# Optimization experiments

Measured on AMD Instinct MI355X. Metric: run time of the kernel, lower is better.

Reference implementation:

```python
import jax, jax.numpy as jnp
import numpy as np

LATENT = 100
INIT_SIZE = 8   # img_size // 4
NUM = 200       # LIF time steps
BETA = 0.95
THR = 1.0
CH_OUT = 3

# snntorch ATan surrogate spike (alpha=2 -> grad = 1/(1+(pi*u)^2))
@jax.custom_vjp
def spike_fn(x):
    return (x > 0).astype(x.dtype)

def _spike_fwd(x):
    return (x > 0).astype(x.dtype), x

def _spike_bwd(x, g):
    return (g / (1.0 + (jnp.pi * x) ** 2),)

spike_fn.defvjp(_spike_fwd, _spike_bwd)

def batchnorm(x, gamma, beta, eps):
    # training-mode BN: batch statistics over (N,H,W), biased variance (as torch)
    mean = x.mean(axis=(0, 2, 3), keepdims=True)
    var = ((x - mean) ** 2).mean(axis=(0, 2, 3), keepdims=True)
    xh = (x - mean) * jax.lax.rsqrt(var + eps)
    return xh * gamma[None, :, None, None] + beta[None, :, None, None]

def upsample2x(x):  # nearest-neighbor, scale 2
    return jnp.repeat(jnp.repeat(x, 2, axis=2), 2, axis=3)

def conv2d(x, w, b):  # 3x3, stride 1, padding 1
    y = jax.lax.conv_general_dilated(x, w, (1, 1), [(1, 1), (1, 1)],
                                     dimension_numbers=("NCHW", "OIHW", "NCHW"))
    return y + b[None, :, None, None]

def leaky_relu(x):
    return jnp.where(x >= 0, x, 0.2 * x)

def setup_inputs() -> dict:
    key = jax.random.key(0)
    ks = jax.random.split(key, 8)
    B = 8
    def n(k, shape, s=0.02):
        return jax.random.normal(k, shape, dtype=jnp.float32) * s
    return {
        "z": jax.random.normal(ks[0], (B, LATENT), dtype=jnp.float32),
        "w_l1": n(ks[1], (LATENT, 128 * INIT_SIZE ** 2)),
        "b_l1": jnp.zeros((128 * INIT_SIZE ** 2,), jnp.float32),
        "g1": jnp.ones((128,), jnp.float32), "be1": jnp.zeros((128,), jnp.float32),
        "w_c1": n(ks[2], (128, NUM * 128, 3, 3), 0.005),
        "b_c1": jnp.zeros((128,), jnp.float32),
        "g2": jnp.ones((128,), jnp.float32), "be2": jnp.zeros((128,), jnp.float32),
        "w_c2": n(ks[3], (64, 128, 3, 3)),
        "b_c2": jnp.zeros((64,), jnp.float32),
        "g3": jnp.ones((64,), jnp.float32), "be3": jnp.zeros((64,), jnp.float32),
        "w_c3": n(ks[4], (CH_OUT, 64, 3, 3)),
        "b_c3": jnp.zeros((CH_OUT,), jnp.float32),
    }

def reference(z, w_l1, b_l1, g1, be1, w_c1, b_c1, g2, be2, w_c2, b_c2, g3, be3, w_c3, b_c3):
    B = z.shape[0]
    out = z @ w_l1 + b_l1                       # (B, 128*8*8)
    out = out.reshape(B, 128, INIT_SIZE, INIT_SIZE)
    out = batchnorm(out, g1, be1, 1e-5)
    out = upsample2x(out)                       # (B,128,16,16) constant LIF input

    def lif_step(mem, _):
        # snntorch Leaky, reset-by-subtraction; reset detached from grad
        reset = jax.lax.stop_gradient((mem > THR).astype(mem.dtype))
        mem = BETA * mem + out - reset * THR
        spk = spike_fn(mem - THR)
        return mem, spk

    mem0 = jnp.zeros_like(out)
    _, spk_rec = jax.lax.scan(lif_step, mem0, None, length=NUM)  # (NUM,B,128,16,16)
    # faithful to torch.stack(dim=0).reshape(B, -1, 16, 16)
    x = spk_rec.reshape(B, NUM * 128, 16, 16)
    x = conv2d(x, w_c1, b_c1)                   # (B,128,16,16)
    x = leaky_relu(batchnorm(x, g2, be2, 0.8))  # BatchNorm2d(128, 0.8): eps=0.8
    x = upsample2x(x)                           # (B,128,32,32)
    x = conv2d(x, w_c2, b_c2)                   # (B,64,32,32)
    x = leaky_relu(batchnorm(x, g3, be3, 0.8))
    x = conv2d(x, w_c3, b_c3)                   # (B,3,32,32)
    return jnp.tanh(x)
```

## Files before the change

### kernel.cpp

```cpp
#include <hip/hip_runtime.h>
#include <math.h>


#define WROW 25632
#define SROW 25664

typedef _Float16 half8 __attribute__((ext_vector_type(8)));
typedef float f32x4 __attribute__((ext_vector_type(4)));
typedef unsigned int uint4v __attribute__((ext_vector_type(4)));

union AFrag { uint4v u4; unsigned int u[4]; half8 h; };

__global__ __launch_bounds__(256) void k_lin_bn1(
    const float* __restrict__ z, const float* __restrict__ w,
    const float* __restrict__ bias, const float* __restrict__ g1,
    const float* __restrict__ be1, float* __restrict__ I) {
  int ch = blockIdx.x, tid = threadIdx.x;
  __shared__ float red[256];
  int hw = tid & 63, b0 = tid >> 6;
  int j = ch * 64 + hw;
  float acc0 = bias[j], acc1 = acc0;
  const float* zp0 = z + b0 * 100;
  const float* zp1 = z + (b0 + 4) * 100;
  for (int l = 0; l < 100; ++l) {
    float wv = w[l * 8192 + j];
    acc0 += zp0[l] * wv;
    acc1 += zp1[l] * wv;
  }
  float v0 = acc0, v1 = acc1;
  red[tid] = v0 + v1; __syncthreads();
  for (int s = 128; s > 0; s >>= 1) { if (tid < s) red[tid] += red[tid + s]; __syncthreads(); }
  float mean = red[0] * (1.0f / 512.0f);
  __syncthreads();
  float d0 = v0 - mean, d1 = v1 - mean;
  red[tid] = d0 * d0 + d1 * d1; __syncthreads();
  for (int s = 128; s > 0; s >>= 1) { if (tid < s) red[tid] += red[tid + s]; __syncthreads(); }
  float var = red[0] * (1.0f / 512.0f);
  float coef = g1[ch] / sqrtf(var + 1e-5f);
  float beta = be1[ch];
  float q0 = (v0 - mean) * coef + beta;
  float q1 = (v1 - mean) * coef + beta;
#pragma unroll
  for (int k = 0; k < 2; ++k) {
    int n = k ? (tid + 256) : tid; float q = k ? q1 : q0;
    int b = n >> 6, hh = n & 63, h = hh >> 3, ww = hh & 7;
    float* o = I + (size_t)(b * 128 + ch) * 256 + (2 * h) * 16 + 2 * ww;
    o[0] = q; o[1] = q; o[16] = q; o[17] = q;
  }
}

__global__ __launch_bounds__(256) void k_lif(
    const float* __restrict__ I, unsigned char* __restrict__ spkTb) {
  int g = blockIdx.x * 256 + threadIdx.x;
  if (g < 217600) {
    int hr = g / 3200;
    int i  = g - hr * 3200;
    int row;
    if (hr < 18)      row = hr;
    else if (hr < 36) row = 306 + (hr - 18);
    else { int kk = hr - 36; row = ((kk >> 1) + 1) * 18 + ((kk & 1) ? 17 : 0); }
    *(unsigned long long*)(spkTb + (size_t)row * SROW + (size_t)i * 8) = 0ULL;
  }
  int px = g >> 10, plane = g & 1023;
  int lane = threadIdx.x & 63;
  float in = I[plane * 256 + px];
  int pos = ((px >> 4) + 1) * 18 + (px & 15) + 1;
  unsigned long long* wsrow =
      (unsigned long long*)(spkTb + (size_t)pos * SROW + ((plane - lane) >> 3));
  float mem = 0.0f;
  for (int t = 0; t < 200; ++t) {
    float reset = (mem > 1.0f) ? 1.0f : 0.0f;
    mem = 0.95f * mem + in - reset;
    unsigned long long m = __ballot(mem > 1.0f);
    if (lane == 0) wsrow[t * 16] = m;
  }
}

__global__ __launch_bounds__(256) void k_wtrans(
    const float* __restrict__ wc1, _Float16* __restrict__ wT) {
  __shared__ float t[2][2304];
  int op = blockIdx.x / 100, cg = blockIdx.x % 100;
  int oc0 = op * 2, c0 = cg * 256, tid = threadIdx.x;
  const float* src = wc1 + (size_t)oc0 * 230400 + (size_t)c0 * 9;
#pragma unroll
  for (int i = 0; i < 9; ++i) {
    t[0][tid + i * 256] = src[tid + i * 256];
    t[1][tid + i * 256] = src[230400 + tid + i * 256];
  }
  __syncthreads();
  int oh = tid >> 7;
  int cp = tid & 127;
#pragma unroll
  for (int tap = 0; tap < 9; ++tap) {
    union { unsigned int u; _Float16 h[2]; } pk;
    pk.h[0] = (_Float16)t[oh][(2 * cp) * 9 + tap];
    pk.h[1] = (_Float16)t[oh][(2 * cp + 1) * 9 + tap];
    *(unsigned int*)((char*)wT +
        ((size_t)(tap * 128 + oc0 + oh) * WROW + c0 + 2 * cp) * 2) = pk.u;
  }
}

__device__ inline void expandp(unsigned int b, AFrag& f) {
  unsigned int lo = ((b & 0xFu) * 0x00204081u) & 0x01010101u;
  unsigned int hi = ((b >> 4) * 0x00204081u) & 0x01010101u;
  lo *= 0x3Cu; hi *= 0x3Cu;
  f.u[0] = __builtin_amdgcn_perm(0u, lo, 0x01040004u);
  f.u[1] = __builtin_amdgcn_perm(0u, lo, 0x03040204u);
  f.u[2] = __builtin_amdgcn_perm(0u, hi, 0x01040004u);
  f.u[3] = __builtin_amdgcn_perm(0u, hi, 0x03040204u);
}

__device__ __forceinline__ void gll16(const void* g, void* l) {
  __builtin_amdgcn_global_load_lds(
      (const __attribute__((address_space(1))) unsigned int*)g,
      (__attribute__((address_space(3))) unsigned int*)l, 16, 0, 0);
}

__global__ __launch_bounds__(256, 3) void k_conv1_mfma(
    const unsigned char* __restrict__ spkTb, const _Float16* __restrict__ wT,
    _Float16* __restrict__ y1p) {
  int v = (blockIdx.x & 7) * 96 + (blockIdx.x >> 3);
  int sl = v >> 4;
  int r = v & 15;
  int half = r >> 3, b = r & 7;
  int tid = threadIdx.x;
  int wave = tid >> 6, lane = tid & 63;
  int quad = lane >> 4, l16 = lane & 15;
  int qs = quad * 8;
  int h0 = wave * 4;

  int q0 = (sl * 25) / 6;
  int qc = ((sl + 1) * 25) / 6 - q0;
  int NBS = 9 * qc;

  __shared__ _Float16 As[2][8192];

  int ocl = tid >> 4;
  int sc0 = (tid & 15) ^ ocl;
  const char* srcA0 = (const char*)wT + (size_t)q0 * 256
                    + (size_t)(half * 64 + ocl) * (WROW * 2) + sc0 * 16;

  const unsigned char* rowp[4];
#pragma unroll
  for (int nt = 0; nt < 4; ++nt)
    rowp[nt] = spkTb + b * 3200 + q0 * 16
             + (size_t)((h0 + nt) * 18 + l16) * SROW;

  int dsb[4];
#pragma unroll
  for (int s = 0; s < 4; ++s)
    dsb[s] = l16 * 256 + ((s * 64 + quad * 16) ^ (l16 << 4));

  f32x4 acc[4][4] = {};

#pragma unroll
  for (int i = 0; i < 4; ++i)
    gll16(srcA0 + (size_t)i * (16 * WROW * 2), (char*)As + i * 4096 + wave * 1024);
  __syncthreads();

  int tap = 0, qi = 0;
  for (int k = 0; k < NBS; ++k) {
    int dh = tap / 3, dw = tap - dh * 3;
    uint4v bx[4];
    int boff = (dh * 18 + dw) * SROW + qi * 16;
#pragma unroll
    for (int nt = 0; nt < 4; ++nt)
      bx[nt] = *(const uint4v*)(rowp[nt] + boff);
    int qin = qi + 1, tapn = tap;
    if (qin == qc) { qin = 0; tapn = tap + 1; }
    if (k + 1 < NBS) {
      size_t aoff = (size_t)tapn * ((size_t)128 * WROW * 2) + (size_t)qin * 256;
      char* dst = (char*)As + ((k + 1) & 1) * 16384 + wave * 1024;
#pragma unroll
      for (int i = 0; i < 4; ++i)
        gll16(srcA0 + (size_t)i * (16 * WROW * 2) + aoff, dst + i * 4096);
    }
    const char* cA = (const char*)As + (k & 1) * 16384;
#pragma unroll
    for (int s = 0; s < 4; ++s) {
      AFrag a[4];
#pragma unroll
      for (int mt = 0; mt < 4; ++mt)
        a[mt].u4 = *(const uint4v*)(cA + dsb[s] + mt * 4096);
#pragma unroll
      for (int nt = 0; nt < 4; ++nt) {
        AFrag bf; expandp((bx[nt][s] >> qs) & 0xFFu, bf);
#pragma unroll
        for (int mt = 0; mt < 4; ++mt)
          acc[mt][nt] = __builtin_amdgcn_mfma_f32_16x16x32_f16(
              a[mt].h, bf.h, acc[mt][nt], 0, 0, 0);
      }
    }
    __syncthreads();
    tap = tapn; qi = qin;
  }

  _Float16* ob = y1p + (size_t)(sl * 8 + b) * 32768 + half * 16384;
#pragma unroll
  for (int mt = 0; mt < 4; ++mt)
#pragma unroll
    for (int nt = 0; nt < 4; ++nt) {
      int px = (h0 + nt) * 16 + l16;
#pragma unroll
      for (int rr = 0; rr < 4; ++rr) {
        int oc = mt * 16 + quad * 4 + rr;
        ob[(size_t)oc * 256 + px] = (_Float16)acc[mt][nt][rr];
      }
    }
}

__global__ __launch_bounds__(256) void k_bn2_up(
    const _Float16* __restrict__ y1p, const float* __restrict__ bc1,
    const float* __restrict__ g2, const float* __restrict__ be2,
    float* __restrict__ x2p) {
  int ch = blockIdx.x, tid = threadIdx.x;
  __shared__ float red[256];

  for (int e = tid; e < 1056; e += 256) {
    int b = e / 132, i = e - b * 132;
    int rr, cc;
    if (i < 34)       { rr = 0;       cc = i; }
    else if (i < 68)  { rr = 33;      cc = i - 34; }
    else if (i < 100) { rr = i - 67;  cc = 0; }
    else              { rr = i - 99;  cc = 33; }
    x2p[(size_t)(b * 128 + ch) * 1156 + rr * 34 + cc] = 0.0f;
  }

  int pp = tid & 127;
  int bh = tid >> 7;
  float bias = bc1[ch];
  float a[4][2] = {};
  const char* base = (const char*)y1p + ((size_t)ch * 256 + pp * 2) * 2
                   + (size_t)bh * 4 * 65536;
  for (int tl = 0; tl < 48; ++tl) {
    const char* q = base + (size_t)tl * 524288;
#pragma unroll
    for (int k = 0; k < 4; ++k) {
      union { unsigned int u; _Float16 h[2]; } cv;
      cv.u = *(const unsigned int*)(q + (size_t)k * 65536);
      a[k][0] += (float)cv.h[0];
      a[k][1] += (float)cv.h[1];
    }
  }
  float vv[4][2]; float s = 0.0f;
#pragma unroll
  for (int k = 0; k < 4; ++k)
#pragma unroll
    for (int e = 0; e < 2; ++e) { vv[k][e] = a[k][e] + bias; s += vv[k][e]; }

  red[tid] = s; __syncthreads();
  for (int st = 128; st > 0; st >>= 1) { if (tid < st) red[tid] += red[tid + st]; __syncthreads(); }
  float mean = red[0] * (1.0f / 2048.0f);
  __syncthreads();
  s = 0.0f;
#pragma unroll
  for (int k = 0; k < 4; ++k)
#pragma unroll
    for (int e = 0; e < 2; ++e) { float d = vv[k][e] - mean; s += d * d; }
  red[tid] = s; __syncthreads();
  for (int st = 128; st > 0; st >>= 1) { if (tid < st) red[tid] += red[tid + st]; __syncthreads(); }
  float var = red[0] * (1.0f / 2048.0f);
  float coef = g2[ch] / sqrtf(var + 0.8f);
  float beta = be2[ch];
#pragma unroll
  for (int k = 0; k < 4; ++k)
#pragma unroll
    for (int e = 0; e < 2; ++e) {
      int b = bh * 4 + k, px = pp * 2 + e, h = px >> 4, w = px & 15;
      float q = (vv[k][e] - mean) * coef + beta;
      q = (q >= 0.0f) ? q : 0.2f * q;
      float* o = x2p + (size_t)(b * 128 + ch) * 1156 + (2 * h + 1) * 34 + (2 * w + 1);
      o[0] = q; o[1] = q; o[34] = q; o[35] = q;
    }
}

__global__ __launch_bounds__(256) void k_conv2(
    const float* __restrict__ x2p, const float* __restrict__ wc2,
    const float* __restrict__ bc2, float* __restrict__ y2) {
  int b = blockIdx.x & 7;
  int rem = blockIdx.x >> 3;
  int octile = rem >> 2, pq = rem & 3;
  int tid = threadIdx.x;
  int p = pq * 256 + tid, h = p >> 5, w = p & 31;
  float a0 = 0.0f, a1 = 0.0f, a2 = 0.0f, a3 = 0.0f;
  const float* base = x2p + (size_t)(b * 128) * 1156 + h * 34 + w;
  const float* wb = wc2 + (size_t)(octile * 4) * 128 * 9;
  for (int ch = 0; ch < 128; ++ch) {
    const float* pp = base + (size_t)ch * 1156;
    float s0 = pp[0],  s1 = pp[1],  s2 = pp[2];
    float s3 = pp[34], s4 = pp[35], s5 = pp[36];
    float s6 = pp[68], s7 = pp[69], s8 = pp[70];
    const float* w0 = wb + (size_t)ch * 9;
    const float* w1 = wb + (size_t)(128 + ch) * 9;
    const float* w2 = wb + (size_t)(256 + ch) * 9;
    const float* w3 = wb + (size_t)(384 + ch) * 9;
    a0 += s0*w0[0]+s1*w0[1]+s2*w0[2]+s3*w0[3]+s4*w0[4]+s5*w0[5]+s6*w0[6]+s7*w0[7]+s8*w0[8];
    a1 += s0*w1[0]+s1*w1[1]+s2*w1[2]+s3*w1[3]+s4*w1[4]+s5*w1[5]+s6*w1[6]+s7*w1[7]+s8*w1[8];
    a2 += s0*w2[0]+s1*w2[1]+s2*w2[2]+s3*w2[3]+s4*w2[4]+s5*w2[5]+s6*w2[6]+s7*w2[7]+s8*w2[8];
    a3 += s0*w3[0]+s1*w3[1]+s2*w3[2]+s3*w3[3]+s4*w3[4]+s5*w3[5]+s6*w3[6]+s7*w3[7]+s8*w3[8];
  }
  int oc0 = octile * 4;
  y2[(size_t)(b * 64 + oc0 + 0) * 1024 + p] = a0 + bc2[oc0 + 0];
  y2[(size_t)(b * 64 + oc0 + 1) * 1024 + p] = a1 + bc2[oc0 + 1];
  y2[(size_t)(b * 64 + oc0 + 2) * 1024 + p] = a2 + bc2[oc0 + 2];
  y2[(size_t)(b * 64 + oc0 + 3) * 1024 + p] = a3 + bc2[oc0 + 3];
}

__global__ __launch_bounds__(256) void k_bn3(
    const float* __restrict__ y2, const float* __restrict__ g3,
    const float* __restrict__ be3, float* __restrict__ y2n) {
  int ch = blockIdx.x, tid = threadIdx.x;
  __shared__ float red[256];

  for (int e = tid; e < 1056; e += 256) {
    int b = e / 132, i = e - b * 132;
    int rr, cc;
    if (i < 34)       { rr = 0;       cc = i; }
    else if (i < 68)  { rr = 33;      cc = i - 34; }
    else if (i < 100) { rr = i - 67;  cc = 0; }
    else              { rr = i - 99;  cc = 33; }
    y2n[(size_t)(b * 64 + ch) * 1156 + rr * 34 + cc] = 0.0f;
  }

  float v[32]; float s = 0.0f;
#pragma unroll
  for (int k = 0; k < 32; ++k) {
    int n = tid + k * 256;
    v[k] = y2[(size_t)((n >> 10) * 64 + ch) * 1024 + (n & 1023)];
    s += v[k];
  }
  red[tid] = s; __syncthreads();
  for (int st = 128; st > 0; st >>= 1) { if (tid < st) red[tid] += red[tid + st]; __syncthreads(); }
  float mean = red[0] * (1.0f / 8192.0f);
  __syncthreads();
  s = 0.0f;
#pragma unroll
  for (int k = 0; k < 32; ++k) { float d = v[k] - mean; s += d * d; }
  red[tid] = s; __syncthreads();
  for (int st = 128; st > 0; st >>= 1) { if (tid < st) red[tid] += red[tid + st]; __syncthreads(); }
  float var = red[0] * (1.0f / 8192.0f);
  float coef = g3[ch] / sqrtf(var + 0.8f);
  float beta = be3[ch];
#pragma unroll
  for (int k = 0; k < 32; ++k) {
    int n = tid + k * 256;
    int b = n >> 10, px = n & 1023, h = px >> 5, w = px & 31;
    float q = (v[k] - mean) * coef + beta;
    q = (q >= 0.0f) ? q : 0.2f * q;
    y2n[(size_t)(b * 64 + ch) * 1156 + (h + 1) * 34 + (w + 1)] = q;
  }
}

__global__ __launch_bounds__(256) void k_conv3(
    const float* __restrict__ y2n, const float* __restrict__ wc3,
    const float* __restrict__ bc3, float* __restrict__ out) {
  int b = blockIdx.x & 7, pg = blockIdx.x >> 3;
  int tid = threadIdx.x;
  int pxl = tid & 63, cg = tid >> 6;
  int p = pg * 64 + pxl, h = p >> 5, w = p & 31;
  float a0 = 0.0f, a1 = 0.0f, a2 = 0.0f;
  const float* base = y2n + (size_t)(b * 64 + cg * 16) * 1156 + h * 34 + w;
  for (int c = 0; c < 16; ++c) {
    int ch = cg * 16 + c;
    const float* pp = base + (size_t)c * 1156;
    float s0 = pp[0],  s1 = pp[1],  s2 = pp[2];
    float s3 = pp[34], s4 = pp[35], s5 = pp[36];
    float s6 = pp[68], s7 = pp[69], s8 = pp[70];
    const float* w0 = wc3 + (size_t)ch * 9;
    const float* w1 = wc3 + (size_t)(64 + ch) * 9;
    const float* w2 = wc3 + (size_t)(128 + ch) * 9;
    a0 += s0*w0[0]+s1*w0[1]+s2*w0[2]+s3*w0[3]+s4*w0[4]+s5*w0[5]+s6*w0[6]+s7*w0[7]+s8*w0[8];
    a1 += s0*w1[0]+s1*w1[1]+s2*w1[2]+s3*w1[3]+s4*w1[4]+s5*w1[5]+s6*w1[6]+s7*w1[7]+s8*w1[8];
    a2 += s0*w2[0]+s1*w2[1]+s2*w2[2]+s3*w2[3]+s4*w2[4]+s5*w2[5]+s6*w2[6]+s7*w2[7]+s8*w2[8];
  }
  __shared__ float red[3][256];
  red[0][tid] = a0; red[1][tid] = a1; red[2][tid] = a2;
  __syncthreads();
  if (tid < 192) {
    int oc = tid >> 6, px = tid & 63;
    float sres = red[oc][px] + red[oc][px + 64] + red[oc][px + 128] + red[oc][px + 192];
    out[(size_t)(b * 3 + oc) * 1024 + pg * 64 + px] = tanhf(sres + bc3[oc]);
  }
}

extern "C" void kernel_launch(void* const* d_in, const int* in_sizes, int n_in,
                              void* d_out, int out_size, void* d_ws, size_t ws_size,
                              hipStream_t stream) {
  const float* z    = (const float*)d_in[0];
  const float* w_l1 = (const float*)d_in[1];
  const float* b_l1 = (const float*)d_in[2];
  const float* g1   = (const float*)d_in[3];
  const float* be1  = (const float*)d_in[4];
  const float* w_c1 = (const float*)d_in[5];
  const float* b_c1 = (const float*)d_in[6];
  const float* g2   = (const float*)d_in[7];
  const float* be2  = (const float*)d_in[8];
  const float* w_c2 = (const float*)d_in[9];
  const float* b_c2 = (const float*)d_in[10];
  const float* g3   = (const float*)d_in[11];
  const float* be3  = (const float*)d_in[12];
  const float* w_c3 = (const float*)d_in[13];
  const float* b_c3 = (const float*)d_in[14];
  float* out = (float*)d_out;

  char* ws = (char*)d_ws;
  _Float16* wT = (_Float16*)ws;
  unsigned char* spkTb = (unsigned char*)(ws + 59056128);
  float* I   = (float*)(ws + 67633408);
  _Float16* y1p = (_Float16*)(ws + 69730560);
  float* x2p = (float*)ws;
  float* y2n = (float*)(ws + 4734976);
  float* y2  = (float*)(ws + 7102464);

  k_wtrans <<<6400, 256, 0, stream>>>(w_c1, wT);
  k_lin_bn1<<<128, 256, 0, stream>>>(z, w_l1, b_l1, g1, be1, I);
  k_lif    <<<1024, 256, 0, stream>>>(I, spkTb);
  k_conv1_mfma<<<768, 256, 0, stream>>>(spkTb, wT, y1p);

  k_bn2_up <<<128, 256, 0, stream>>>(y1p, b_c1, g2, be2, x2p);
  k_conv2  <<<512, 256, 0, stream>>>(x2p, w_c2, b_c2, y2);
  k_bn3    <<<64, 256, 0, stream>>>(y2, g3, be3, y2n);
  k_conv3  <<<128, 256, 0, stream>>>(y2n, w_c3, b_c3, out);
}
```

Before: 430.8 us.

## Merge weight transpose with linear+BN1, fuse BN3 stats into conv2 and conv3

Folds the conv1 weight-transpose kernel and the linear+BN1 kernel into a single launch that splits work by block index. BN3 is removed as a separate pass: conv2 accumulates per-channel sum and sum-of-squares with wave shuffles and atomics, and conv3 applies normalization and leaky ReLU on the fly with bounds checks instead of reading a padded buffer. This drops two launches and one full read/write of the conv2 output. In exchange it adds atomic contention, computes variance as E[x^2]-mean^2 (less numerically stable), and repeats the BN math inside conv3.

```diff
diff --git a/kernel.cpp b/kernel.cpp
--- a/kernel.cpp
+++ b/kernel.cpp
@@ -11,41 +11,68 @@
 
 union AFrag { uint4v u4; unsigned int u[4]; half8 h; };
 
-__global__ __launch_bounds__(256) void k_lin_bn1(
-    const float* __restrict__ z, const float* __restrict__ w,
-    const float* __restrict__ bias, const float* __restrict__ g1,
+__global__ __launch_bounds__(256) void k_pre(
+    const float* __restrict__ wc1, _Float16* __restrict__ wT,
+    const float* __restrict__ z, const float* __restrict__ wl1,
+    const float* __restrict__ bl1, const float* __restrict__ g1,
     const float* __restrict__ be1, float* __restrict__ I) {
-  int ch = blockIdx.x, tid = threadIdx.x;
-  __shared__ float red[256];
-  int hw = tid & 63, b0 = tid >> 6;
-  int j = ch * 64 + hw;
-  float acc0 = bias[j], acc1 = acc0;
-  const float* zp0 = z + b0 * 100;
-  const float* zp1 = z + (b0 + 4) * 100;
-  for (int l = 0; l < 100; ++l) {
-    float wv = w[l * 8192 + j];
-    acc0 += zp0[l] * wv;
-    acc1 += zp1[l] * wv;
-  }
-  float v0 = acc0, v1 = acc1;
-  red[tid] = v0 + v1; __syncthreads();
-  for (int s = 128; s > 0; s >>= 1) { if (tid < s) red[tid] += red[tid + s]; __syncthreads(); }
-  float mean = red[0] * (1.0f / 512.0f);
-  __syncthreads();
-  float d0 = v0 - mean, d1 = v1 - mean;
-  red[tid] = d0 * d0 + d1 * d1; __syncthreads();
-  for (int s = 128; s > 0; s >>= 1) { if (tid < s) red[tid] += red[tid + s]; __syncthreads(); }
-  float var = red[0] * (1.0f / 512.0f);
-  float coef = g1[ch] / sqrtf(var + 1e-5f);
-  float beta = be1[ch];
-  float q0 = (v0 - mean) * coef + beta;
-  float q1 = (v1 - mean) * coef + beta;
-#pragma unroll
-  for (int k = 0; k < 2; ++k) {
-    int n = k ? (tid + 256) : tid; float q = k ? q1 : q0;
-    int b = n >> 6, hh = n & 63, h = hh >> 3, ww = hh & 7;
-    float* o = I + (size_t)(b * 128 + ch) * 256 + (2 * h) * 16 + 2 * ww;
-    o[0] = q; o[1] = q; o[16] = q; o[17] = q;
+  __shared__ float smem[4608];
+  int tid = threadIdx.x;
+  if (blockIdx.x < 128) {
+    int ch = blockIdx.x;
+    float* red = smem;
+    int hw = tid & 63, b0 = tid >> 6;
+    int j = ch * 64 + hw;
+    float acc0 = bl1[j], acc1 = acc0;
+    const float* zp0 = z + b0 * 100;
+    const float* zp1 = z + (b0 + 4) * 100;
+    for (int l = 0; l < 100; ++l) {
+      float wv = wl1[l * 8192 + j];
+      acc0 += zp0[l] * wv;
+      acc1 += zp1[l] * wv;
+    }
+    float v0 = acc0, v1 = acc1;
+    red[tid] = v0 + v1; __syncthreads();
+    for (int s = 128; s > 0; s >>= 1) { if (tid < s) red[tid] += red[tid + s]; __syncthreads(); }
+    float mean = red[0] * (1.0f / 512.0f);
+    __syncthreads();
+    float d0 = v0 - mean, d1 = v1 - mean;
+    red[tid] = d0 * d0 + d1 * d1; __syncthreads();
+    for (int s = 128; s > 0; s >>= 1) { if (tid < s) red[tid] += red[tid + s]; __syncthreads(); }
+    float var = red[0] * (1.0f / 512.0f);
+    float coef = g1[ch] / sqrtf(var + 1e-5f);
+    float beta = be1[ch];
+    float q0 = (v0 - mean) * coef + beta;
+    float q1 = (v1 - mean) * coef + beta;
+#pragma unroll
+    for (int k = 0; k < 2; ++k) {
+      int n = k ? (tid + 256) : tid; float q = k ? q1 : q0;
+      int b = n >> 6, hh = n & 63, h = hh >> 3, ww = hh & 7;
+      float* o = I + (size_t)(b * 128 + ch) * 256 + (2 * h) * 16 + 2 * ww;
+      o[0] = q; o[1] = q; o[16] = q; o[17] = q;
+    }
+  } else {
+    int wid = blockIdx.x - 128;
+    float (*t)[2304] = (float(*)[2304])smem;
+    int op = wid / 100, cg = wid % 100;
+    int oc0 = op * 2, c0 = cg * 256;
+    const float* src = wc1 + (size_t)oc0 * 230400 + (size_t)c0 * 9;
+#pragma unroll
+    for (int i = 0; i < 9; ++i) {
+      t[0][tid + i * 256] = src[tid + i * 256];
+      t[1][tid + i * 256] = src[230400 + tid + i * 256];
+    }
+    __syncthreads();
+    int oh = tid >> 7;
+    int cp = tid & 127;
+#pragma unroll
+    for (int tap = 0; tap < 9; ++tap) {
+      union { unsigned int u; _Float16 h[2]; } pk;
+      pk.h[0] = (_Float16)t[oh][(2 * cp) * 9 + tap];
+      pk.h[1] = (_Float16)t[oh][(2 * cp + 1) * 9 + tap];
+      *(unsigned int*)((char*)wT +
+          ((size_t)(tap * 128 + oc0 + oh) * WROW + c0 + 2 * cp) * 2) = pk.u;
+    }
   }
 }
 
@@ -76,30 +103,6 @@
   }
 }
 
-__global__ __launch_bounds__(256) void k_wtrans(
-    const float* __restrict__ wc1, _Float16* __restrict__ wT) {
-  __shared__ float t[2][2304];
-  int op = blockIdx.x / 100, cg = blockIdx.x % 100;
-  int oc0 = op * 2, c0 = cg * 256, tid = threadIdx.x;
-  const float* src = wc1 + (size_t)oc0 * 230400 + (size_t)c0 * 9;
-#pragma unroll
-  for (int i = 0; i < 9; ++i) {
-    t[0][tid + i * 256] = src[tid + i * 256];
-    t[1][tid + i * 256] = src[230400 + tid + i * 256];
-  }
-  __syncthreads();
-  int oh = tid >> 7;
-  int cp = tid & 127;
-#pragma unroll
-  for (int tap = 0; tap < 9; ++tap) {
-    union { unsigned int u; _Float16 h[2]; } pk;
-    pk.h[0] = (_Float16)t[oh][(2 * cp) * 9 + tap];
-    pk.h[1] = (_Float16)t[oh][(2 * cp + 1) * 9 + tap];
-    *(unsigned int*)((char*)wT +
-        ((size_t)(tap * 128 + oc0 + oh) * WROW + c0 + 2 * cp) * 2) = pk.u;
-  }
-}
-
 __device__ inline void expandp(unsigned int b, AFrag& f) {
   unsigned int lo = ((b & 0xFu) * 0x00204081u) & 0x01010101u;
   unsigned int hi = ((b >> 4) * 0x00204081u) & 0x01010101u;
@@ -212,9 +215,11 @@
 __global__ __launch_bounds__(256) void k_bn2_up(
     const _Float16* __restrict__ y1p, const float* __restrict__ bc1,
     const float* __restrict__ g2, const float* __restrict__ be2,
-    float* __restrict__ x2p) {
+    float* __restrict__ x2p, float* __restrict__ stats) {
   int ch = blockIdx.x, tid = threadIdx.x;
   __shared__ float red[256];
+
+  if (blockIdx.x == 0 && tid < 128) stats[tid] = 0.0f;
 
   for (int e = tid; e < 1056; e += 256) {
     int b = e / 132, i = e - b * 132;
@@ -276,7 +281,8 @@
 
 __global__ __launch_bounds__(256) void k_conv2(
     const float* __restrict__ x2p, const float* __restrict__ wc2,
-    const float* __restrict__ bc2, float* __restrict__ y2) {
+    const float* __restrict__ bc2, float* __restrict__ y2,
+    float* __restrict__ stats) {
   int b = blockIdx.x & 7;
   int rem = blockIdx.x >> 3;
   int octile = rem >> 2, pq = rem & 3;
@@ -300,78 +306,73 @@
     a3 += s0*w3[0]+s1*w3[1]+s2*w3[2]+s3*w3[3]+s4*w3[4]+s5*w3[5]+s6*w3[6]+s7*w3[7]+s8*w3[8];
   }
   int oc0 = octile * 4;
-  y2[(size_t)(b * 64 + oc0 + 0) * 1024 + p] = a0 + bc2[oc0 + 0];
-  y2[(size_t)(b * 64 + oc0 + 1) * 1024 + p] = a1 + bc2[oc0 + 1];
-  y2[(size_t)(b * 64 + oc0 + 2) * 1024 + p] = a2 + bc2[oc0 + 2];
-  y2[(size_t)(b * 64 + oc0 + 3) * 1024 + p] = a3 + bc2[oc0 + 3];
-}
-
-__global__ __launch_bounds__(256) void k_bn3(
-    const float* __restrict__ y2, const float* __restrict__ g3,
-    const float* __restrict__ be3, float* __restrict__ y2n) {
-  int ch = blockIdx.x, tid = threadIdx.x;
-  __shared__ float red[256];
-
-  for (int e = tid; e < 1056; e += 256) {
-    int b = e / 132, i = e - b * 132;
-    int rr, cc;
-    if (i < 34)       { rr = 0;       cc = i; }
-    else if (i < 68)  { rr = 33;      cc = i - 34; }
-    else if (i < 100) { rr = i - 67;  cc = 0; }
-    else              { rr = i - 99;  cc = 33; }
-    y2n[(size_t)(b * 64 + ch) * 1156 + rr * 34 + cc] = 0.0f;
-  }
-
-  float v[32]; float s = 0.0f;
-#pragma unroll
-  for (int k = 0; k < 32; ++k) {
-    int n = tid + k * 256;
-    v[k] = y2[(size_t)((n >> 10) * 64 + ch) * 1024 + (n & 1023)];
-    s += v[k];
-  }
-  red[tid] = s; __syncthreads();
-  for (int st = 128; st > 0; st >>= 1) { if (tid < st) red[tid] += red[tid + st]; __syncthreads(); }
-  float mean = red[0] * (1.0f / 8192.0f);
+  float v0 = a0 + bc2[oc0 + 0];
+  float v1 = a1 + bc2[oc0 + 1];
+  float v2 = a2 + bc2[oc0 + 2];
+  float v3 = a3 + bc2[oc0 + 3];
+  y2[(size_t)(b * 64 + oc0 + 0) * 1024 + p] = v0;
+  y2[(size_t)(b * 64 + oc0 + 1) * 1024 + p] = v1;
+  y2[(size_t)(b * 64 + oc0 + 2) * 1024 + p] = v2;
+  y2[(size_t)(b * 64 + oc0 + 3) * 1024 + p] = v3;
+  float q0 = v0 * v0, q1 = v1 * v1, q2 = v2 * v2, q3 = v3 * v3;
+#pragma unroll
+  for (int off = 32; off > 0; off >>= 1) {
+    v0 += __shfl_down(v0, off); q0 += __shfl_down(q0, off);
+    v1 += __shfl_down(v1, off); q1 += __shfl_down(q1, off);
+    v2 += __shfl_down(v2, off); q2 += __shfl_down(q2, off);
+    v3 += __shfl_down(v3, off); q3 += __shfl_down(q3, off);
+  }
+  if ((tid & 63) == 0) {
+    atomicAdd(&stats[oc0 + 0], v0); atomicAdd(&stats[64 + oc0 + 0], q0);
+    atomicAdd(&stats[oc0 + 1], v1); atomicAdd(&stats[64 + oc0 + 1], q1);
+    atomicAdd(&stats[oc0 + 2], v2); atomicAdd(&stats[64 + oc0 + 2], q2);
+    atomicAdd(&stats[oc0 + 3], v3); atomicAdd(&stats[64 + oc0 + 3], q3);
+  }
+}
+
+__global__ __launch_bounds__(256) void k_conv3(
+    const float* __restrict__ y2, const float* __restrict__ stats,
+    const float* __restrict__ g3, const float* __restrict__ be3,
+    const float* __restrict__ wc3, const float* __restrict__ bc3,
+    float* __restrict__ out) {
+  __shared__ float cA[64], cB[64];
+  int tid = threadIdx.x;
+  if (tid < 64) {
+    float mean = stats[tid] * (1.0f / 8192.0f);
+    float var = stats[64 + tid] * (1.0f / 8192.0f) - mean * mean;
+    float coef = g3[tid] / sqrtf(var + 0.8f);
+    cA[tid] = coef;
+    cB[tid] = be3[tid] - mean * coef;
+  }
   __syncthreads();
-  s = 0.0f;
-#pragma unroll
-  for (int k = 0; k < 32; ++k) { float d = v[k] - mean; s += d * d; }
-  red[tid] = s; __syncthreads();
-  for (int st = 128; st > 0; st >>= 1) { if (tid < st) red[tid] += red[tid + st]; __syncthreads(); }
-  float var = red[0] * (1.0f / 8192.0f);
-  float coef = g3[ch] / sqrtf(var + 0.8f);
-  float beta = be3[ch];
-#pragma unroll
-  for (int k = 0; k < 32; ++k) {
-    int n = tid + k * 256;
-    int b = n >> 10, px = n & 1023, h = px >> 5, w = px & 31;
-    float q = (v[k] - mean) * coef + beta;
-    q = (q >= 0.0f) ? q : 0.2f * q;
-    y2n[(size_t)(b * 64 + ch) * 1156 + (h + 1) * 34 + (w + 1)] = q;
-  }
-}
-
-__global__ __launch_bounds__(256) void k_conv3(
-    const float* __restrict__ y2n, const float* __restrict__ wc3,
-    const float* __restrict__ bc3, float* __restrict__ out) {
   int b = blockIdx.x & 7, pg = blockIdx.x >> 3;
-  int tid = threadIdx.x;
   int pxl = tid & 63, cg = tid >> 6;
   int p = pg * 64 + pxl, h = p >> 5, w = p & 31;
   float a0 = 0.0f, a1 = 0.0f, a2 = 0.0f;
-  const float* base = y2n + (size_t)(b * 64 + cg * 16) * 1156 + h * 34 + w;
+  const float* ybase = y2 + (size_t)(b * 64 + cg * 16) * 1024;
   for (int c = 0; c < 16; ++c) {
     int ch = cg * 16 + c;
-    const float* pp = base + (size_t)c * 1156;
-    float s0 = pp[0],  s1 = pp[1],  s2 = pp[2];
-    float s3 = pp[34], s4 = pp[35], s5 = pp[36];
-    float s6 = pp[68], s7 = pp[69], s8 = pp[70];
+    const float* pl = ybase + (size_t)c * 1024;
+    float ca = cA[ch], cb = cB[ch];
+    float s[9];
+#pragma unroll
+    for (int dh = 0; dh < 3; ++dh)
+#pragma unroll
+      for (int dwi = 0; dwi < 3; ++dwi) {
+        int hh = h + dh - 1, ww = w + dwi - 1;
+        float v = 0.0f;
+        if (hh >= 0 && hh < 32 && ww >= 0 && ww < 32) {
+          float t = pl[hh * 32 + ww] * ca + cb;
+          v = (t >= 0.0f) ? t : 0.2f * t;
+        }
+        s[dh * 3 + dwi] = v;
+      }
     const float* w0 = wc3 + (size_t)ch * 9;
     const float* w1 = wc3 + (size_t)(64 + ch) * 9;
     const float* w2 = wc3 + (size_t)(128 + ch) * 9;
-    a0 += s0*w0[0]+s1*w0[1]+s2*w0[2]+s3*w0[3]+s4*w0[4]+s5*w0[5]+s6*w0[6]+s7*w0[7]+s8*w0[8];
-    a1 += s0*w1[0]+s1*w1[1]+s2*w1[2]+s3*w1[3]+s4*w1[4]+s5*w1[5]+s6*w1[6]+s7*w1[7]+s8*w1[8];
-    a2 += s0*w2[0]+s1*w2[1]+s2*w2[2]+s3*w2[3]+s4*w2[4]+s5*w2[5]+s6*w2[6]+s7*w2[7]+s8*w2[8];
+    a0 += s[0]*w0[0]+s[1]*w0[1]+s[2]*w0[2]+s[3]*w0[3]+s[4]*w0[4]+s[5]*w0[5]+s[6]*w0[6]+s[7]*w0[7]+s[8]*w0[8];
+    a1 += s[0]*w1[0]+s[1]*w1[1]+s[2]*w1[2]+s[3]*w1[3]+s[4]*w1[4]+s[5]*w1[5]+s[6]*w1[6]+s[7]*w1[7]+s[8]*w1[8];
+    a2 += s[0]*w2[0]+s[1]*w2[1]+s[2]*w2[2]+s[3]*w2[3]+s[4]*w2[4]+s[5]*w2[5]+s[6]*w2[6]+s[7]*w2[7]+s[8]*w2[8];
   }
   __shared__ float red[3][256];
   red[0][tid] = a0; red[1][tid] = a1; red[2][tid] = a2;
@@ -408,17 +409,15 @@
   unsigned char* spkTb = (unsigned char*)(ws + 59056128);
   float* I   = (float*)(ws + 67633408);
   _Float16* y1p = (_Float16*)(ws + 69730560);
-  float* x2p = (float*)ws;
-  float* y2n = (float*)(ws + 4734976);
-  float* y2  = (float*)(ws + 7102464);
-
-  k_wtrans <<<6400, 256, 0, stream>>>(w_c1, wT);
-  k_lin_bn1<<<128, 256, 0, stream>>>(z, w_l1, b_l1, g1, be1, I);
+  float* x2p   = (float*)ws;
+  float* y2    = (float*)(ws + 4734976);
+  float* stats = (float*)(ws + 6832128);
+
+  k_pre    <<<6528, 256, 0, stream>>>(w_c1, wT, z, w_l1, b_l1, g1, be1, I);
   k_lif    <<<1024, 256, 0, stream>>>(I, spkTb);
   k_conv1_mfma<<<768, 256, 0, stream>>>(spkTb, wT, y1p);
 
-  k_bn2_up <<<128, 256, 0, stream>>>(y1p, b_c1, g2, be2, x2p);
-  k_conv2  <<<512, 256, 0, stream>>>(x2p, w_c2, b_c2, y2);
-  k_bn3    <<<64, 256, 0, stream>>>(y2, g3, be3, y2n);
-  k_conv3  <<<128, 256, 0, stream>>>(y2n, w_c3, b_c3, out);
-}
+  k_bn2_up <<<128, 256, 0, stream>>>(y1p, b_c1, g2, be2, x2p, stats);
+  k_conv2  <<<512, 256, 0, stream>>>(x2p, w_c2, b_c2, y2, stats);
+  k_conv3  <<<128, 256, 0, stream>>>(y2, stats, g3, be3, w_c3, b_c3, out);
+}
```

Measured after the change: 486.6 us. 1.13x slower.
